# Kernel tuning notes

Measured on AMD Instinct MI355X. Metric: run time of the kernel, lower is better.

Reference implementation:

```python
import jax, jax.numpy as jnp
import numpy as np

HEADS = 6
FILTERS = (16, 32, 64)
V_FEATS = 11
N_NODES = 30000
N_EDGES = 480000


def setup_inputs() -> dict:
    key = jax.random.key(0)
    ks = jax.random.split(key, 20)
    d = {}
    d["x_int"] = jax.random.normal(ks[0], (N_NODES, V_FEATS), jnp.float32)
    d["x_nh"] = jax.random.normal(ks[1], (N_NODES, V_FEATS), jnp.float32)
    d["ei_int"] = jax.random.randint(ks[2], (2, N_EDGES), 0, N_NODES, jnp.int32)
    d["ei_nh"] = jax.random.randint(ks[3], (2, N_EDGES), 0, N_NODES, jnp.int32)
    f_in = V_FEATS
    kidx = 4
    for i, f in enumerate(FILTERS, 1):
        s = 1.0 / np.sqrt(f_in)
        d[f"W{i}"] = (jax.random.normal(ks[kidx], (f_in, HEADS * f), jnp.float32) * s); kidx += 1
        sa = 1.0 / np.sqrt(f)
        d[f"a{i}s"] = (jax.random.normal(ks[kidx], (HEADS, f), jnp.float32) * sa); kidx += 1
        d[f"a{i}d"] = (jax.random.normal(ks[kidx], (HEADS, f), jnp.float32) * sa); kidx += 1
        f_in = HEADS * f
    d["Wd"] = jax.random.normal(ks[kidx], (2 * HEADS * FILTERS[-1], 1), jnp.float32) * 0.05
    d["bd"] = jnp.zeros((1,), jnp.float32)
    return d


def _gat_layer(h, src, dst, W, a_s, a_d):
    """One multi-head graph-attention (DGAT) layer, heads concatenated.
    h: [N, F_in]; W: [F_in, H*F_out]; a_s, a_d: [H, F_out]."""
    N = h.shape[0]
    H, Fo = a_s.shape
    z = (h @ W).reshape(N, H, Fo)                      # [N, H, Fo]
    e_src = jnp.einsum('nhf,hf->nh', z, a_s)           # [N, H]
    e_dst = jnp.einsum('nhf,hf->nh', z, a_d)
    e = jax.nn.leaky_relu(e_src[src] + e_dst[dst], 0.2)  # [E, H]
    # softmax over incoming edges of each destination node
    e_max = jax.ops.segment_max(e, dst, num_segments=N)  # [N, H] (-inf for empty)
    ex = jnp.exp(e - e_max[dst])
    denom = jax.ops.segment_sum(ex, dst, num_segments=N)
    alpha = ex / (denom[dst] + 1e-16)                   # [E, H]
    msg = z[src] * alpha[:, :, None]                    # [E, H, Fo]
    out = jax.ops.segment_sum(msg, dst, num_segments=N) # [N, H, Fo]
    return jax.nn.elu(out).reshape(N, H * Fo)


def reference(x_int, x_nh, W1, a1s, a1d, W2, a2s, a2d, W3, a3s, a3d, Wd, bd, ei_int, ei_nh):
    layers = [(W1, a1s, a1d), (W2, a2s, a2d), (W3, a3s, a3d)]

    def run(h, ei):
        src, dst = ei[0], ei[1]
        for (W, a_s, a_d) in layers:
            h = _gat_layer(h, src, dst, W, a_s, a_d)
        return h

    hi = run(x_int, ei_int)   # [N, 384]
    hn = run(x_nh, ei_nh)     # [N, 384]
    x = jnp.concatenate([hi, hn], axis=1)       # [N, 768]
    x = jnp.sum(x, axis=0).reshape(1, -1)       # [1, 768] sum pooling
    norm = jnp.maximum(jnp.linalg.norm(x, axis=1, keepdims=True), 1e-12)
    x = x / norm                                # F.normalize
    x = x @ Wd + bd                             # Dense, linear nonlin
    return jnp.squeeze(x, 1)                    # [1]
```

## Files before the change

### kernel.cpp

```cpp
#include <hip/hip_runtime.h>
#include <math.h>

#define N_NODES 30000
#define N_EDGES 480000
#define HEADS   6
#define NN2 (2 * N_NODES)
#define NE2 (2 * N_EDGES)

typedef __attribute__((ext_vector_type(8))) short bf16x8;
typedef __attribute__((ext_vector_type(4))) float f32x4;
typedef __attribute__((ext_vector_type(2))) float f32x2;
typedef __attribute__((ext_vector_type(4))) unsigned u32x4;

__device__ __forceinline__ unsigned short f2bf(float f) {
    unsigned u = __float_as_uint(f);
    u += 0x7fffu + ((u >> 16) & 1u);
    return (unsigned short)(u >> 16);
}

__global__ void gemm1_es_kernel(const float* __restrict__ x0, const float* __restrict__ x1,
                                const float* __restrict__ W, const float* __restrict__ a_s,
                                const float* __restrict__ a_d,
                                unsigned char* __restrict__ zf8b, float* __restrict__ es8,
                                float* __restrict__ ed8) {
    constexpr int K = 11, HF = 96, TM = 16, Fo = 16;
    __shared__ float hs[TM * K];
    const int m0 = blockIdx.x * TM;
    const float* h = (m0 < N_NODES) ? (x0 + (size_t)m0 * K)
                                    : (x1 + (size_t)(m0 - N_NODES) * K);
    const int j = blockIdx.y * 64 + threadIdx.x;
    for (int idx = threadIdx.x; idx < TM * K; idx += 64) hs[idx] = h[idx];
    __syncthreads();
    if (j >= HF) return;
    float acc[TM];
#pragma unroll
    for (int m = 0; m < TM; ++m) acc[m] = 0.f;
    for (int k = 0; k < K; ++k) {
        float w = W[k * HF + j];
#pragma unroll
        for (int m = 0; m < TM; ++m) acc[m] = fmaf(hs[m * K + k], w, acc[m]);
    }
    const float as_v = a_s[j];
    const float ad_v = a_d[j];
    const int hh = j >> 4;
    const int fo = j & 15;
#pragma unroll
    for (int m = 0; m < TM; ++m) {
        const int pk = __builtin_amdgcn_cvt_pk_fp8_f32(acc[m], acc[m], 0, false);
        zf8b[((size_t)hh * NN2 + (m0 + m)) * Fo + fo] = (unsigned char)pk;
    }
#pragma unroll
    for (int m = 0; m < TM; ++m) {
        float ep = acc[m] * as_v;
        float dp = acc[m] * ad_v;
#pragma unroll
        for (int d = 1; d < 16; d <<= 1) {
            ep += __shfl_xor(ep, d);
            dp += __shfl_xor(dp, d);
        }
        if ((threadIdx.x & 15) == 0) {
            es8[(size_t)(m0 + m) * 8 + hh] = ep;
            ed8[(size_t)(m0 + m) * 8 + hh] = dp;
        }
    }
}

__global__ void convert_wt_kernel(const float* __restrict__ W, unsigned short* __restrict__ Wt,
                                  int K, int HF) {
    const int idx = blockIdx.x * 256 + threadIdx.x;
    if (idx >= K * HF) return;
    const int k = idx / HF;
    const int n = idx - k * HF;
    Wt[n * K + k] = f2bf(W[idx]);
}

template <int K, int HF>
__global__ __launch_bounds__(256) void gemm_es_kernel(
        const unsigned short* __restrict__ hbf, const unsigned short* __restrict__ Wt,
        const float* __restrict__ a_s, const float* __restrict__ a_d,
        unsigned char* __restrict__ zf8b, float* __restrict__ es8,
        float* __restrict__ ed8) {
    constexpr int KSTEPS = K / 32;
    constexpr int Fo  = HF / HEADS;
    constexpr int TPH = Fo / 16;
    constexpr int NT  = HF / 16;
    constexpr int PAD = 8;
    constexpr int LROW = K + PAD;
    constexpr int NCH = 16 * K / 8;
    __shared__ unsigned short bl[16 * LROW];

    const int tid  = threadIdx.x;
    const int wid  = blockIdx.x * 4 + (tid >> 6);
    const bool active = wid < NN2 / 16;
    const int lane = tid & 63;
    const int r16  = lane & 15;
    const int quad = lane >> 4;
    const int m0 = active ? wid * 16 : 0;

    bf16x8 afrag[KSTEPS];
    const unsigned short* ap = hbf + (size_t)(m0 + r16) * K + quad * 8;
#pragma unroll
    for (int i = 0; i < KSTEPS; ++i) afrag[i] = *(const bf16x8*)(ap + i * 32);

    u32x4 st[2];
#pragma unroll
    for (int j = 0; j < 2; ++j) {
        const int c = tid + j * 256;
        if (c < NCH) st[j] = *(const u32x4*)(Wt + (size_t)c * 8);
    }

    float es_p[4] = {0.f, 0.f, 0.f, 0.f};
    float ed_p[4] = {0.f, 0.f, 0.f, 0.f};
    for (int t = 0; t < NT; ++t) {
        __syncthreads();
#pragma unroll
        for (int j = 0; j < 2; ++j) {
            const int c = tid + j * 256;
            if (c < NCH) {
                const int row = c / (K / 8);
                const int co  = c - row * (K / 8);
                *(u32x4*)(bl + row * LROW + co * 8) = st[j];
            }
        }
        if (t + 1 < NT) {
            const unsigned short* wp = Wt + (size_t)(t + 1) * 16 * K;
#pragma unroll
            for (int j = 0; j < 2; ++j) {
                const int c = tid + j * 256;
                if (c < NCH) st[j] = *(const u32x4*)(wp + (size_t)c * 8);
            }
        }
        __syncthreads();

        f32x4 acc = {0.f, 0.f, 0.f, 0.f};
        const unsigned short* bp = bl + r16 * LROW + quad * 8;
#pragma unroll
        for (int i = 0; i < KSTEPS; ++i) {
            const bf16x8 bfrag = *(const bf16x8*)(bp + i * 32);
            acc = __builtin_amdgcn_mfma_f32_16x16x32_bf16(afrag[i], bfrag, acc, 0, 0, 0);
        }
        const float as_v = a_s[t * 16 + r16];
        const float ad_v = a_d[t * 16 + r16];
        const int th = t / TPH;
        const int fo = (t % TPH) * 16 + r16;
        unsigned char* zp = zf8b + ((size_t)th * NN2 + (m0 + quad * 4)) * Fo + fo;
#pragma unroll
        for (int r = 0; r < 4; ++r) {
            const int pk = __builtin_amdgcn_cvt_pk_fp8_f32(acc[r], acc[r], 0, false);
            if (active) zp[(size_t)r * Fo] = (unsigned char)pk;
            es_p[r] = fmaf(acc[r], as_v, es_p[r]);
            ed_p[r] = fmaf(acc[r], ad_v, ed_p[r]);
        }
        if (((t + 1) % TPH) == 0) {
            const int h = t / TPH;
#pragma unroll
            for (int r = 0; r < 4; ++r) {
                float ep = es_p[r], dp = ed_p[r];
#pragma unroll
                for (int d = 1; d < 16; d <<= 1) {
                    ep += __shfl_xor(ep, d);
                    dp += __shfl_xor(dp, d);
                }
                if (active && r16 == 0) {
                    es8[(size_t)(m0 + quad * 4 + r) * 8 + h] = ep;
                    ed8[(size_t)(m0 + quad * 4 + r) * 8 + h] = dp;
                }
                es_p[r] = 0.f;
                ed_p[r] = 0.f;
            }
        }
    }
}

__global__ void zero_int_kernel(int* __restrict__ p, int n) {
    const int i = blockIdx.x * 256 + threadIdx.x;
    if (i < n) p[i] = 0;
}

__global__ void hist2_kernel(const int* __restrict__ ei0, const int* __restrict__ ei1,
                             int* __restrict__ cnt) {
    const int e = blockIdx.x * 256 + threadIdx.x;
    if (e >= NE2) return;
    const int g = e >= N_EDGES;
    const int* ei = g ? ei1 : ei0;
    const int e2 = e - g * N_EDGES;
    atomicAdd(&cnt[g * N_NODES + ei[N_EDGES + e2]], 1);
}

#define SCAN_NB ((NN2 + 1023) / 1024)
__global__ void scan1_kernel(int* tmp, int* __restrict__ bsum) {
    __shared__ int s[1024];
    const int t = threadIdx.x;
    const int gid = blockIdx.x * 1024 + t;
    const int v = (gid < NN2) ? tmp[gid] : 0;
    s[t] = v;
    __syncthreads();
    for (int d = 1; d < 1024; d <<= 1) {
        int x = (t >= d) ? s[t - d] : 0;
        __syncthreads();
        s[t] += x;
        __syncthreads();
    }
    tmp[gid] = s[t] - v;
    if (t == 1023) bsum[blockIdx.x] = s[1023];
}

__global__ void scan2_kernel(int* __restrict__ bsum, int* __restrict__ boff) {
    if (threadIdx.x == 0) {
        int a = 0;
        for (int i = 0; i < SCAN_NB; ++i) { boff[i] = a; a += bsum[i]; }
        boff[SCAN_NB] = a;
    }
}

__global__ void scan3_kernel(int* tmp, const int* __restrict__ boff,
                             int* __restrict__ off) {
    const int gid = blockIdx.x * 1024 + threadIdx.x;
    if (gid < NN2) {
        const int o = tmp[gid] + boff[gid >> 10];
        off[gid] = o;
        tmp[gid] = o;
    }
    if (gid == 0) off[NN2] = boff[SCAN_NB];
}

__global__ void scatter2_kernel(const int* __restrict__ ei0, const int* __restrict__ ei1,
                                int* __restrict__ cursor,
                                unsigned* __restrict__ csrp) {
    const int e = blockIdx.x * 256 + threadIdx.x;
    if (e >= NE2) return;
    const int g = e >= N_EDGES;
    const int* ei = g ? ei1 : ei0;
    const int e2 = e - g * N_EDGES;
    const int src = g * N_NODES + ei[e2];
    const int dst = g * N_NODES + ei[N_EDGES + e2];
    const int slot = atomicAdd(&cursor[dst], 1);
    csrp[slot] = ((unsigned)dst << 16) | (unsigned)src;
}

__global__ void winsort_kernel(const int* __restrict__ off,
                               unsigned short* __restrict__ sorted) {
    __shared__ unsigned skey[256];
    const int t = threadIdx.x;
    const int n = blockIdx.x * 256 + t;
    unsigned v = 0xFFFFFFFFu;
    if (n < NN2) {
        int deg = off[n + 1] - off[n];
        if (deg > 65535) deg = 65535;
        v = ((unsigned)deg << 16) | ((unsigned)n & 0xFFFFu);
    }
    skey[t] = v;
    for (unsigned k = 2; k <= 256; k <<= 1) {
        for (unsigned j = k >> 1; j > 0; j >>= 1) {
            __syncthreads();
            const unsigned ixj = (unsigned)t ^ j;
            if (ixj > (unsigned)t) {
                const unsigned a = skey[t], b = skey[ixj];
                const bool up = ((t & k) == 0);
                if (up ? (a > b) : (a < b)) { skey[t] = b; skey[ixj] = a; }
            }
        }
    }
    __syncthreads();
    const int pos = blockIdx.x * 256 + t;
    if (pos < NN2) sorted[pos] = (unsigned short)(skey[t] & 0xFFFFu);
}

__global__ __launch_bounds__(256) void edgew_kernel(
        const unsigned* __restrict__ csrp,
        const float* __restrict__ es8, const float* __restrict__ ed8,
        unsigned* __restrict__ pA, unsigned* __restrict__ pB) {
    const int s = blockIdx.x * 256 + threadIdx.x;
    if (s >= NE2) return;
    const unsigned sd = csrp[s];
    const unsigned src = sd & 0xFFFFu;
    const unsigned dst = sd >> 16;
    const f32x4 ea = *(const f32x4*)(es8 + src * 8u);
    const f32x2 eb = *(const f32x2*)(es8 + src * 8u + 4);
    const f32x4 da = *(const f32x4*)(ed8 + dst * 8u);
    const f32x2 db = *(const f32x2*)(ed8 + dst * 8u + 4);
    float ev[6];
    ev[0] = ea.x + da.x; ev[1] = ea.y + da.y; ev[2] = ea.z + da.z;
    ev[3] = ea.w + da.w; ev[4] = eb.x + db.x; ev[5] = eb.y + db.y;
#pragma unroll
    for (int h = 0; h < 6; ++h) {
        float v = ev[h];
        v = fmaxf(v, 0.2f * v);
        const unsigned rec = ((unsigned)f2bf(__expf(v)) << 16) | src;
        unsigned* p = (h < 3) ? (pA + (size_t)h * NE2) : (pB + (size_t)(h - 3) * NE2);
        p[s] = rec;
    }
}

template <int HF, int GS, int MAIN, int G>
__global__ __launch_bounds__(256) void agg_sub_kernel(
        const int* __restrict__ off, const unsigned short* __restrict__ sorted,
        const unsigned* __restrict__ ewA, const unsigned* __restrict__ ewB,
        const unsigned* __restrict__ zf8, unsigned short* __restrict__ outz) {
    constexpr int Fo  = HF / HEADS;
    constexpr int L   = Fo / 4;
    constexpr int EPI = GS / L;
    constexpr int GPW = 64 / GS;
    constexpr int NB  = 4 * GPW;
    constexpr int BPH = NN2 / NB;
    int h, blk;
    {
        const int r = blockIdx.x & 7, g = blockIdx.x >> 3;
        if (r < 6) {
            if (g >= MAIN) return;
            h = r; blk = g;
        } else {
            const int k = (r - 6) * G + g;
            if (k >= 6 * (BPH - MAIN)) return;
            h = k % 6; blk = MAIN + k / 6;
        }
    }
    const int wavid = threadIdx.x >> 6;
    const int lane  = threadIdx.x & 63;
    const int grp = lane / GS;
    const int lg  = lane - grp * GS;
    const int eo = lg / L;
    const int fp = lg - eo * L;
    const int npos = blk * NB + wavid * GPW + grp;
    const int n = sorted[npos];

    const int s0  = off[n];
    const int deg = off[n + 1] - s0;
    const unsigned* ewp = ((h < 3) ? (ewA + (size_t)h * NE2)
                                   : (ewB + (size_t)(h - 3) * NE2)) + s0;
    const unsigned* zh = zf8 + (size_t)h * ((size_t)NN2 * L);

    float a0 = 0.f, a1 = 0.f, a2 = 0.f, a3 = 0.f, lsum = 0.f;
    for (int ib = 0; ib < deg; ib += 4 * EPI) {
        unsigned rec[4];
#pragma unroll
        for (int k = 0; k < 4; ++k) {
            const int idx = ib + k * EPI + eo;
            rec[k] = ewp[idx < deg ? idx : 0];
        }
        unsigned zz[4];
#pragma unroll
        for (int k = 0; k < 4; ++k)
            zz[k] = zh[(rec[k] & 0xFFFFu) * (unsigned)L + (unsigned)fp];
#pragma unroll
        for (int k = 0; k < 4; ++k) {
            const int idx = ib + k * EPI + eo;
            float ww = __uint_as_float(rec[k] & 0xFFFF0000u);
            ww = (idx < deg) ? ww : 0.f;
            lsum += ww;
            const f32x2 lo = __builtin_amdgcn_cvt_pk_f32_fp8((int)zz[k], false);
            const f32x2 hi = __builtin_amdgcn_cvt_pk_f32_fp8((int)zz[k], true);
            a0 = fmaf(ww, lo.x, a0);
            a1 = fmaf(ww, lo.y, a1);
            a2 = fmaf(ww, hi.x, a2);
            a3 = fmaf(ww, hi.y, a3);
        }
    }
#pragma unroll
    for (int d = L; d < GS; d <<= 1) {
        a0 += __shfl_xor(a0, d);
        a1 += __shfl_xor(a1, d);
        a2 += __shfl_xor(a2, d);
        a3 += __shfl_xor(a3, d);
        lsum += __shfl_xor(lsum, d);
    }
    if (eo == 0) {
        const float inv = 1.f / (lsum + 1e-16f);
        float o0 = a0 * inv, o1 = a1 * inv, o2 = a2 * inv, o3 = a3 * inv;
        o0 = o0 > 0.f ? o0 : (__expf(o0) - 1.f);
        o1 = o1 > 0.f ? o1 : (__expf(o1) - 1.f);
        o2 = o2 > 0.f ? o2 : (__expf(o2) - 1.f);
        o3 = o3 > 0.f ? o3 : (__expf(o3) - 1.f);
        unsigned short* op = outz + (size_t)n * HF + h * Fo + 4 * fp;
        *(unsigned*)op       = (unsigned)f2bf(o0) | ((unsigned)f2bf(o1) << 16);
        *(unsigned*)(op + 2) = (unsigned)f2bf(o2) | ((unsigned)f2bf(o3) << 16);
    }
}

#define POOL_BLOCKS 3072
#define POOL_WAVES 2048
__global__ __launch_bounds__(256) void agg_pool_kernel(
        const int* __restrict__ off, const unsigned short* __restrict__ sorted,
        const unsigned* __restrict__ ewA, const unsigned* __restrict__ ewB,
        const unsigned* __restrict__ zf8, float* __restrict__ pooled) {
    __shared__ float lds[128];
    int h, slot;
    {
        const int r = blockIdx.x & 7, g = blockIdx.x >> 3;
        if (r < 6) { h = r; slot = g; }
        else { h = g % 6; slot = 384 + (r - 6) * 64 + g / 6; }
    }
    const int wavid = threadIdx.x >> 6;
    const int ws    = slot * 4 + wavid;
    const int lane  = threadIdx.x & 63;
    const int c  = lane >> 2;
    const int fp = lane & 3;
    const unsigned* ewh = (h < 3) ? (ewA + (size_t)h * NE2)
                                  : (ewB + (size_t)(h - 3) * NE2);
    const u32x4* zq = (const u32x4*)(zf8 + (size_t)h * ((size_t)NN2 * 16));

    if (threadIdx.x < 128) lds[threadIdx.x] = 0.f;
    __syncthreads();

    float p0[16], p1[16];
#pragma unroll
    for (int j = 0; j < 16; ++j) { p0[j] = 0.f; p1[j] = 0.f; }

    for (int base = ws * 16; base < NN2; base += POOL_WAVES * 16) {
        const int npos = base + c;
        const int n = sorted[npos];
        const int s0  = off[n];
        const int deg = off[n + 1] - s0;
        int dmx = deg;
#pragma unroll
        for (int d = 4; d < 64; d <<= 1) {
            const int o = __shfl_xor(dmx, d);
            dmx = o > dmx ? o : dmx;
        }
        const unsigned* ewp = ewh + s0;
        float acc[16];
#pragma unroll
        for (int j = 0; j < 16; ++j) acc[j] = 0.f;
        float lsum = 0.f;
        for (int ib = 0; ib < dmx; ib += 4) {
            unsigned rec[4];
#pragma unroll
            for (int k = 0; k < 4; ++k) {
                const int idx = ib + k;
                rec[k] = ewp[idx < deg ? idx : 0];
            }
            u32x4 zz[4];
#pragma unroll
            for (int k = 0; k < 4; ++k)
                zz[k] = zq[(rec[k] & 0xFFFFu) * 4u + (unsigned)fp];
#pragma unroll
            for (int k = 0; k < 4; ++k) {
                float w = __uint_as_float(rec[k] & 0xFFFF0000u);
                w = ((ib + k) < deg) ? w : 0.f;
                lsum += w;
#pragma unroll
                for (int d = 0; d < 4; ++d) {
                    const f32x2 lo = __builtin_amdgcn_cvt_pk_f32_fp8((int)zz[k][d], false);
                    const f32x2 hi = __builtin_amdgcn_cvt_pk_f32_fp8((int)zz[k][d], true);
                    acc[4 * d + 0] = fmaf(w, lo.x, acc[4 * d + 0]);
                    acc[4 * d + 1] = fmaf(w, lo.y, acc[4 * d + 1]);
                    acc[4 * d + 2] = fmaf(w, hi.x, acc[4 * d + 2]);
                    acc[4 * d + 3] = fmaf(w, hi.y, acc[4 * d + 3]);
                }
            }
        }
        {
            const float inv = 1.f / (lsum + 1e-16f);
            if (n < N_NODES) {
#pragma unroll
                for (int j = 0; j < 16; ++j) {
                    float o = acc[j] * inv;
                    o = o > 0.f ? o : (__expf(o) - 1.f);
                    p0[j] += o;
                }
            } else {
#pragma unroll
                for (int j = 0; j < 16; ++j) {
                    float o = acc[j] * inv;
                    o = o > 0.f ? o : (__expf(o) - 1.f);
                    p1[j] += o;
                }
            }
        }
    }
#pragma unroll
    for (int d = 4; d < 64; d <<= 1) {
#pragma unroll
        for (int j = 0; j < 16; ++j) {
            p0[j] += __shfl_xor(p0[j], d);
            p1[j] += __shfl_xor(p1[j], d);
        }
    }
    if (lane < 4) {
#pragma unroll
        for (int j = 0; j < 16; ++j) {
            atomicAdd(&lds[fp * 16 + j], p0[j]);
            atomicAdd(&lds[64 + fp * 16 + j], p1[j]);
        }
    }
    __syncthreads();
    if (threadIdx.x < 128) {
        const int g2 = threadIdx.x >> 6;
        const int f  = threadIdx.x & 63;
        atomicAdd(&pooled[g2 * 384 + h * 64 + f], lds[threadIdx.x]);
    }
}

__global__ void zero_pooled_kernel(float* __restrict__ p) {
    const int i = blockIdx.x * 256 + threadIdx.x;
    if (i < 768) p[i] = 0.f;
}

__global__ void final_kernel(const float* __restrict__ pooled, const float* __restrict__ Wd,
                             const float* __restrict__ bd, float* __restrict__ outp) {
    __shared__ float s_ss[256], s_dot[256];
    const int t = threadIdx.x;
    float ss = 0.f, dot = 0.f;
    for (int c = t; c < 768; c += 256) {
        const float v = pooled[c];
        ss  = fmaf(v, v, ss);
        dot = fmaf(v, Wd[c], dot);
    }
    s_ss[t] = ss; s_dot[t] = dot;
    __syncthreads();
    for (int off = 128; off > 0; off >>= 1) {
        if (t < off) { s_ss[t] += s_ss[t + off]; s_dot[t] += s_dot[t + off]; }
        __syncthreads();
    }
    if (t == 0) {
        const float norm = fmaxf(sqrtf(s_ss[0]), 1e-12f);
        outp[0] = s_dot[0] / norm + bd[0];
    }
}

extern "C" void kernel_launch(void* const* d_in, const int* in_sizes, int n_in,
                              void* d_out, int out_size, void* d_ws, size_t ws_size,
                              hipStream_t stream) {
    const float* x_int = (const float*)d_in[0];
    const float* x_nh  = (const float*)d_in[1];
    const int*   ei_int = (const int*)d_in[2];
    const int*   ei_nh  = (const int*)d_in[3];
    const float* W1  = (const float*)d_in[4];
    const float* a1s = (const float*)d_in[5];
    const float* a1d = (const float*)d_in[6];
    const float* W2  = (const float*)d_in[7];
    const float* a2s = (const float*)d_in[8];
    const float* a2d = (const float*)d_in[9];
    const float* W3  = (const float*)d_in[10];
    const float* a3s = (const float*)d_in[11];
    const float* a3d = (const float*)d_in[12];
    const float* Wd  = (const float*)d_in[13];
    const float* bd  = (const float*)d_in[14];
    float* out = (float*)d_out;

    unsigned short* hbf_a = (unsigned short*)d_ws;
    unsigned short* hbf_b = hbf_a + (size_t)NN2 * 96;
    unsigned short* wt2   = hbf_b + (size_t)NN2 * 192;
    unsigned short* wt3   = wt2   + (size_t)96 * 192;
    unsigned* zf8 = (unsigned*)(wt3 + (size_t)192 * 384);
    float* es8   = (float*)(zf8 + (size_t)NN2 * 96);
    float* ed8   = es8 + (size_t)NN2 * 8;
    float* pooled = ed8 + (size_t)NN2 * 8;
    int* tmp     = (int*)(pooled + 768);
    int* bsum    = tmp + SCAN_NB * 1024;
    int* boff    = bsum + SCAN_NB;
    int* off     = boff + SCAN_NB + 1;
    unsigned* csrp = (unsigned*)(off + NN2 + 1);
    unsigned short* sorted = (unsigned short*)(csrp + NE2);
    unsigned char* zf8b = (unsigned char*)zf8;

    unsigned* ew13A = (unsigned*)hbf_b;
    unsigned* ew13B = ew13A + (size_t)3 * NE2;
    unsigned* ew2A  = (unsigned*)hbf_a;
    unsigned* ew2B  = zf8 + (size_t)NN2 * 48;

    zero_pooled_kernel<<<3, 256, 0, stream>>>(pooled);
    convert_wt_kernel<<<(96 * 192 + 255) / 256, 256, 0, stream>>>(W2, wt2, 96, 192);
    convert_wt_kernel<<<(192 * 384 + 255) / 256, 256, 0, stream>>>(W3, wt3, 192, 384);

    zero_int_kernel<<<(NN2 + 255) / 256, 256, 0, stream>>>(tmp, NN2);
    hist2_kernel<<<(NE2 + 255) / 256, 256, 0, stream>>>(ei_int, ei_nh, tmp);
    scan1_kernel<<<SCAN_NB, 1024, 0, stream>>>(tmp, bsum);
    scan2_kernel<<<1, 64, 0, stream>>>(bsum, boff);
    scan3_kernel<<<SCAN_NB, 1024, 0, stream>>>(tmp, boff, off);
    scatter2_kernel<<<(NE2 + 255) / 256, 256, 0, stream>>>(ei_int, ei_nh, tmp, csrp);

    winsort_kernel<<<(NN2 + 255) / 256, 256, 0, stream>>>(off, sorted);

    const int mfma_blocks = (NN2 / 16 + 3) / 4;
    const int ew_blocks = (NE2 + 255) / 256;

    gemm1_es_kernel<<<dim3(NN2 / 16, 2), 64, 0, stream>>>(x_int, x_nh, W1, a1s, a1d, zf8b,
                                                          es8, ed8);
    edgew_kernel<<<ew_blocks, 256, 0, stream>>>(csrp, es8, ed8, ew13A, ew13B);
    agg_sub_kernel<96, 16, 2812, 2814><<<8 * 2814, 256, 0, stream>>>(off, sorted, ew13A,
                                                                     ew13B, zf8, hbf_a);
    gemm_es_kernel<96, 192><<<mfma_blocks, 256, 0, stream>>>(hbf_a, wt2, a2s, a2d, zf8b,
                                                             es8, ed8);
    edgew_kernel<<<ew_blocks, 256, 0, stream>>>(csrp, es8, ed8, ew2A, ew2B);
    agg_sub_kernel<192, 32, 5625, 5625><<<45000, 256, 0, stream>>>(off, sorted, ew2A,
                                                                   ew2B, zf8, hbf_b);
    gemm_es_kernel<192, 384><<<mfma_blocks, 256, 0, stream>>>(hbf_b, wt3, a3s, a3d, zf8b,
                                                              es8, ed8);
    edgew_kernel<<<ew_blocks, 256, 0, stream>>>(csrp, es8, ed8, ew13A, ew13B);
    agg_pool_kernel<<<POOL_BLOCKS, 256, 0, stream>>>(off, sorted, ew13A, ew13B, zf8,
                                                     pooled);

    final_kernel<<<1, 256, 0, stream>>>(pooled, Wd, bd, out);
}
```

Measured before the change: 495.6 us.

## Remap aggregation so each lane group owns a node with 16-byte feature loads

The sub-layer aggregation kernel is restructured so a small group of lanes (Fo/16) handles one destination node sequentially over its edges, each lane loading 16 fp8 features as a u32x4 and accumulating 16 outputs. This replaces the previous scheme, which split each node's edges across lanes and then combined them with shuffle reductions. The intent is to remove the shuffle reductions, issue wider memory loads and cut the grid size. In exchange, each lane walks every edge of its node serially, so high-degree nodes make lanes within a wave diverge in loop length, and each lane holds more registers.

```diff
diff --git a/kernel.cpp b/kernel.cpp
--- a/kernel.cpp
+++ b/kernel.cpp
@@ -292,88 +292,83 @@
     }
 }
 
-template <int HF, int GS, int MAIN, int G>
+template <int HF, int G>
 __global__ __launch_bounds__(256) void agg_sub_kernel(
         const int* __restrict__ off, const unsigned short* __restrict__ sorted,
         const unsigned* __restrict__ ewA, const unsigned* __restrict__ ewB,
         const unsigned* __restrict__ zf8, unsigned short* __restrict__ outz) {
     constexpr int Fo  = HF / HEADS;
-    constexpr int L   = Fo / 4;
-    constexpr int EPI = GS / L;
-    constexpr int GPW = 64 / GS;
-    constexpr int NB  = 4 * GPW;
-    constexpr int BPH = NN2 / NB;
-    int h, blk;
-    {
-        const int r = blockIdx.x & 7, g = blockIdx.x >> 3;
-        if (r < 6) {
-            if (g >= MAIN) return;
-            h = r; blk = g;
-        } else {
-            const int k = (r - 6) * G + g;
-            if (k >= 6 * (BPH - MAIN)) return;
-            h = k % 6; blk = MAIN + k / 6;
-        }
-    }
+    constexpr int LPC = Fo / 16;
+    constexpr int CPW = 64 / LPC;
+    constexpr int NB  = 4 * CPW;
+    const int r = blockIdx.x & 7, g = blockIdx.x >> 3;
+    if (r >= 6) return;
+    const int h = r;
     const int wavid = threadIdx.x >> 6;
     const int lane  = threadIdx.x & 63;
-    const int grp = lane / GS;
-    const int lg  = lane - grp * GS;
-    const int eo = lg / L;
-    const int fp = lg - eo * L;
-    const int npos = blk * NB + wavid * GPW + grp;
-    const int n = sorted[npos];
-
-    const int s0  = off[n];
-    const int deg = off[n + 1] - s0;
+    const int c  = lane / LPC;
+    const int fp = lane - c * LPC;
+    const int npos = g * NB + wavid * CPW + c;
+    const bool act = npos < NN2;
+    const int n = act ? (int)sorted[npos] : 0;
+    int s0 = 0, deg = 0;
+    if (act) { s0 = off[n]; deg = off[n + 1] - s0; }
+
     const unsigned* ewp = ((h < 3) ? (ewA + (size_t)h * NE2)
                                    : (ewB + (size_t)(h - 3) * NE2)) + s0;
-    const unsigned* zh = zf8 + (size_t)h * ((size_t)NN2 * L);
-
-    float a0 = 0.f, a1 = 0.f, a2 = 0.f, a3 = 0.f, lsum = 0.f;
-    for (int ib = 0; ib < deg; ib += 4 * EPI) {
+    const u32x4* zq = (const u32x4*)(zf8 + (size_t)h * ((size_t)NN2 * (Fo / 4)));
+
+    float acc[16];
+#pragma unroll
+    for (int j = 0; j < 16; ++j) acc[j] = 0.f;
+    float lsum = 0.f;
+    for (int ib = 0; ib < deg; ib += 4) {
         unsigned rec[4];
 #pragma unroll
         for (int k = 0; k < 4; ++k) {
-            const int idx = ib + k * EPI + eo;
+            const int idx = ib + k;
             rec[k] = ewp[idx < deg ? idx : 0];
         }
-        unsigned zz[4];
+        u32x4 zz[4];
 #pragma unroll
         for (int k = 0; k < 4; ++k)
-            zz[k] = zh[(rec[k] & 0xFFFFu) * (unsigned)L + (unsigned)fp];
+            zz[k] = zq[(rec[k] & 0xFFFFu) * (unsigned)LPC + (unsigned)fp];
 #pragma unroll
         for (int k = 0; k < 4; ++k) {
-            const int idx = ib + k * EPI + eo;
-            float ww = __uint_as_float(rec[k] & 0xFFFF0000u);
-            ww = (idx < deg) ? ww : 0.f;
-            lsum += ww;
-            const f32x2 lo = __builtin_amdgcn_cvt_pk_f32_fp8((int)zz[k], false);
-            const f32x2 hi = __builtin_amdgcn_cvt_pk_f32_fp8((int)zz[k], true);
-            a0 = fmaf(ww, lo.x, a0);
-            a1 = fmaf(ww, lo.y, a1);
-            a2 = fmaf(ww, hi.x, a2);
-            a3 = fmaf(ww, hi.y, a3);
-        }
-    }
-#pragma unroll
-    for (int d = L; d < GS; d <<= 1) {
-        a0 += __shfl_xor(a0, d);
-        a1 += __shfl_xor(a1, d);
-        a2 += __shfl_xor(a2, d);
-        a3 += __shfl_xor(a3, d);
-        lsum += __shfl_xor(lsum, d);
-    }
-    if (eo == 0) {
+            float w = __uint_as_float(rec[k] & 0xFFFF0000u);
+            w = ((ib + k) < deg) ? w : 0.f;
+            lsum += w;
+#pragma unroll
+            for (int d = 0; d < 4; ++d) {
+                const f32x2 lo = __builtin_amdgcn_cvt_pk_f32_fp8((int)zz[k][d], false);
+                const f32x2 hi = __builtin_amdgcn_cvt_pk_f32_fp8((int)zz[k][d], true);
+                acc[4 * d + 0] = fmaf(w, lo.x, acc[4 * d + 0]);
+                acc[4 * d + 1] = fmaf(w, lo.y, acc[4 * d + 1]);
+                acc[4 * d + 2] = fmaf(w, hi.x, acc[4 * d + 2]);
+                acc[4 * d + 3] = fmaf(w, hi.y, acc[4 * d + 3]);
+            }
+        }
+    }
+    if (act) {
         const float inv = 1.f / (lsum + 1e-16f);
-        float o0 = a0 * inv, o1 = a1 * inv, o2 = a2 * inv, o3 = a3 * inv;
-        o0 = o0 > 0.f ? o0 : (__expf(o0) - 1.f);
-        o1 = o1 > 0.f ? o1 : (__expf(o1) - 1.f);
-        o2 = o2 > 0.f ? o2 : (__expf(o2) - 1.f);
-        o3 = o3 > 0.f ? o3 : (__expf(o3) - 1.f);
-        unsigned short* op = outz + (size_t)n * HF + h * Fo + 4 * fp;
-        *(unsigned*)op       = (unsigned)f2bf(o0) | ((unsigned)f2bf(o1) << 16);
-        *(unsigned*)(op + 2) = (unsigned)f2bf(o2) | ((unsigned)f2bf(o3) << 16);
+        float o[16];
+#pragma unroll
+        for (int j = 0; j < 16; ++j) {
+            float v = acc[j] * inv;
+            o[j] = v > 0.f ? v : (__expf(v) - 1.f);
+        }
+        u32x4 v0, v1;
+        v0.x = (unsigned)f2bf(o[0])  | ((unsigned)f2bf(o[1])  << 16);
+        v0.y = (unsigned)f2bf(o[2])  | ((unsigned)f2bf(o[3])  << 16);
+        v0.z = (unsigned)f2bf(o[4])  | ((unsigned)f2bf(o[5])  << 16);
+        v0.w = (unsigned)f2bf(o[6])  | ((unsigned)f2bf(o[7])  << 16);
+        v1.x = (unsigned)f2bf(o[8])  | ((unsigned)f2bf(o[9])  << 16);
+        v1.y = (unsigned)f2bf(o[10]) | ((unsigned)f2bf(o[11]) << 16);
+        v1.z = (unsigned)f2bf(o[12]) | ((unsigned)f2bf(o[13]) << 16);
+        v1.w = (unsigned)f2bf(o[14]) | ((unsigned)f2bf(o[15]) << 16);
+        unsigned short* op = outz + (size_t)n * HF + h * Fo + fp * 16;
+        *(u32x4*)op       = v0;
+        *(u32x4*)(op + 8) = v1;
     }
 }
 
@@ -578,13 +573,13 @@
     gemm1_es_kernel<<<dim3(NN2 / 16, 2), 64, 0, stream>>>(x_int, x_nh, W1, a1s, a1d, zf8b,
                                                           es8, ed8);
     edgew_kernel<<<ew_blocks, 256, 0, stream>>>(csrp, es8, ed8, ew13A, ew13B);
-    agg_sub_kernel<96, 16, 2812, 2814><<<8 * 2814, 256, 0, stream>>>(off, sorted, ew13A,
-                                                                     ew13B, zf8, hbf_a);
+    agg_sub_kernel<96, 235><<<8 * 235, 256, 0, stream>>>(off, sorted, ew13A, ew13B,
+                                                         zf8, hbf_a);
     gemm_es_kernel<96, 192><<<mfma_blocks, 256, 0, stream>>>(hbf_a, wt2, a2s, a2d, zf8b,
                                                              es8, ed8);
     edgew_kernel<<<ew_blocks, 256, 0, stream>>>(csrp, es8, ed8, ew2A, ew2B);
-    agg_sub_kernel<192, 32, 5625, 5625><<<45000, 256, 0, stream>>>(off, sorted, ew2A,
-                                                                   ew2B, zf8, hbf_b);
+    agg_sub_kernel<192, 469><<<8 * 469, 256, 0, stream>>>(off, sorted, ew2A, ew2B,
+                                                          zf8, hbf_b);
     gemm_es_kernel<192, 384><<<mfma_blocks, 256, 0, stream>>>(hbf_b, wt3, a3s, a3d, zf8b,
                                                               es8, ed8);
     edgew_kernel<<<ew_blocks, 256, 0, stream>>>(csrp, es8, ed8, ew13A, ew13B);
```

After: 532.0 us. 1.07x slower.
